# Kernel optimization log

Measured on AMD Instinct MI355X. Metric: run time of the kernel, lower is better.

## Reference

```python
import jax, jax.numpy as jnp
import numpy as np

B, L, J, D_MODEL, N_HIDDEN = 8, 2048, 2048, 1024, 1024


def setup_inputs() -> dict:
    key = jax.random.key(0)
    ks = jax.random.split(key, 6)
    scale = 1.0 / np.sqrt(D_MODEL)
    return {
        "q": jax.random.normal(ks[0], (B, L, D_MODEL), dtype=jnp.float32),
        "k": jax.random.normal(ks[1], (B, J, D_MODEL), dtype=jnp.float32),
        "v": jax.random.normal(ks[2], (B, J, D_MODEL), dtype=jnp.float32),
        "mask": jnp.zeros((B, L, J), dtype=jnp.float32),
        # Linear(d_model, n_hidden, bias=False) weights, stored [n_hidden, d_model] like torch
        "W_q": jax.random.normal(ks[3], (N_HIDDEN, D_MODEL), dtype=jnp.float32) * scale,
        "W_k": jax.random.normal(ks[4], (N_HIDDEN, D_MODEL), dtype=jnp.float32) * scale,
        "W_v": jax.random.normal(ks[5], (N_HIDDEN, D_MODEL), dtype=jnp.float32) * scale,
    }


def reference(q, k, v, mask, W_q, W_k, W_v):
    # Linear projections (torch Linear: x @ W.T)
    qp = jnp.einsum('bld,hd->blh', q, W_q)
    kp = jnp.einsum('bjd,hd->bjh', k, W_k)
    vp = jnp.einsum('bjd,hd->bjh', v, W_v)
    # scaled dot-product scores [B, L, J]
    scores = jnp.einsum('blh,bjh->blj', qp, kp) / jnp.sqrt(jnp.float32(N_HIDDEN)).astype(qp.dtype)
    scores = scores + mask
    attn = jax.nn.softmax(scores, axis=-1)
    return jnp.einsum('blj,bjh->blh', attn, vp)
```

## Files before the change

kernel.cpp:

```cpp
#include <hip/hip_runtime.h>
#include <hip/hip_fp16.h>

typedef _Float16 f16;
typedef __attribute__((ext_vector_type(8))) _Float16 f16x8;
typedef __attribute__((ext_vector_type(4))) _Float16 f16x4;
typedef __attribute__((ext_vector_type(4))) float f32x4;

#define BM 256
#define BN 256
#define BK 32

__device__ __forceinline__ void gll16(const void* src, void* dst) {
  __builtin_amdgcn_global_load_lds((const __attribute__((address_space(1))) void*)src,
                                   (__attribute__((address_space(3))) void*)dst,
                                   16, 0, 0);
}

template<int MODE>
__global__ __launch_bounds__(512, 2)
void gemm_bt(const f16* __restrict__ Aall, const f16* __restrict__ Ball,
             void* __restrict__ Call,
             int M, int N, int K, int lda, int ldb, int ldc,
             long strideA, long strideB, long strideC,
             const float* __restrict__ maskAll, long strideMask,
             float* __restrict__ lvec, float scale)
{
  __shared__ f16 smA[3][BM * BK];
  __shared__ f16 smB[3][BN * BK];

  const int z = blockIdx.z;
  const f16* A = Aall + (long)z * strideA;
  const f16* B = Ball + (long)z * strideB;

  const int tid  = threadIdx.x;
  const int wid  = tid >> 6;
  const int lane = tid & 63;
  const int wm = wid >> 2;
  const int wn = wid & 3;
  const int lr = lane & 15;
  const int g  = lane >> 4;
  const int xc = (lr & 3) ^ ((lr >> 2) & 3);

  const long brow = (long)blockIdx.y * BM;
  const long bcol = (long)blockIdx.x * BN;
  const int  nt   = K / BK;

  f32x4 acc[8][4] = {};

  auto stageA = [&](int buf, int t) {
    #pragma unroll
    for (int i = 0; i < 2; ++i) {
      int c   = i * 512 + tid;
      int row = c >> 2;
      int sl  = (c & 3) ^ ((row & 3) ^ ((row >> 2) & 3));
      gll16(A + (brow + row) * (long)lda + t * BK + sl * 8, &smA[buf][c * 8]);
    }
  };
  auto stageB = [&](int buf, int t) {
    #pragma unroll
    for (int i = 0; i < 2; ++i) {
      int c   = i * 512 + tid;
      int row = c >> 2;
      int sl  = (c & 3) ^ ((row & 3) ^ ((row >> 2) & 3));
      gll16(B + (bcol + row) * (long)ldb + t * BK + sl * 8, &smB[buf][c * 8]);
    }
  };

  stageA(0, 0); stageB(0, 0);
  stageA(1, 1); stageB(1, 1);
  asm volatile("s_waitcnt vmcnt(4)" ::: "memory");
  __builtin_amdgcn_s_barrier();

  int buf = 0;
  for (int kt = 0; kt < nt; ++kt) {
    int bufn = buf + 2; if (bufn >= 3) bufn -= 3;
    const f16* sa = &smA[buf][0];
    const f16* sb = &smB[buf][0];

    f16x8 af[4], bf[4];
    #pragma unroll
    for (int n = 0; n < 4; ++n) {
      int row = wn * 64 + n * 16 + lr;
      bf[n] = *(const f16x8*)(sb + row * BK + (g ^ xc) * 8);
    }
    #pragma unroll
    for (int m = 0; m < 4; ++m) {
      int row = wm * 128 + m * 16 + lr;
      af[m] = *(const f16x8*)(sa + row * BK + (g ^ xc) * 8);
    }
    if (kt + 2 < nt) stageA(bufn, kt + 2);
    __builtin_amdgcn_s_barrier();
    asm volatile("s_waitcnt lgkmcnt(0)" ::: "memory");
    __builtin_amdgcn_sched_barrier(0);
    __builtin_amdgcn_s_setprio(1);
    #pragma unroll
    for (int m = 0; m < 4; ++m)
      #pragma unroll
      for (int n = 0; n < 4; ++n)
        acc[m][n] = __builtin_amdgcn_mfma_f32_16x16x32_f16(af[m], bf[n], acc[m][n], 0, 0, 0);
    __builtin_amdgcn_s_setprio(0);
    __builtin_amdgcn_s_barrier();

    #pragma unroll
    for (int m = 0; m < 4; ++m) {
      int row = wm * 128 + 64 + m * 16 + lr;
      af[m] = *(const f16x8*)(sa + row * BK + (g ^ xc) * 8);
    }
    if (kt + 2 < nt) stageB(bufn, kt + 2);
    __builtin_amdgcn_s_barrier();
    asm volatile("s_waitcnt lgkmcnt(0)" ::: "memory");
    __builtin_amdgcn_sched_barrier(0);
    __builtin_amdgcn_s_setprio(1);
    #pragma unroll
    for (int m = 0; m < 4; ++m)
      #pragma unroll
      for (int n = 0; n < 4; ++n)
        acc[m + 4][n] = __builtin_amdgcn_mfma_f32_16x16x32_f16(af[m], bf[n], acc[m + 4][n], 0, 0, 0);
    __builtin_amdgcn_s_setprio(0);
    __builtin_amdgcn_sched_barrier(0);
    if (kt + 2 < nt) { asm volatile("s_waitcnt vmcnt(4)" ::: "memory"); }
    else             { asm volatile("s_waitcnt vmcnt(0)" ::: "memory"); }
    __builtin_amdgcn_s_barrier();
    buf = buf + 1 == 3 ? 0 : buf + 1;
  }

  const int rb = (lane >> 4) * 4;

  if (MODE == 0) {
    f16* C = (f16*)Call + (long)z * strideC;
    #pragma unroll
    for (int m = 0; m < 8; ++m)
      #pragma unroll
      for (int j = 0; j < 4; ++j) {
        long grow = brow + wm * 128 + m * 16 + rb + j;
        #pragma unroll
        for (int n = 0; n < 4; ++n) {
          long gcol = bcol + wn * 64 + n * 16 + lr;
          C[grow * ldc + gcol] = (f16)acc[m][n][j];
        }
      }
  } else if (MODE == 1) {
    f16* C = (f16*)Call + (long)z * strideC;
    const float* mask = maskAll + (long)z * strideMask;
    #pragma unroll
    for (int m = 0; m < 8; ++m)
      #pragma unroll
      for (int j = 0; j < 4; ++j) {
        long grow = brow + wm * 128 + m * 16 + rb + j;
        float s = 0.f;
        #pragma unroll
        for (int n = 0; n < 4; ++n) {
          long gcol = bcol + wn * 64 + n * 16 + lr;
          float p = __expf(acc[m][n][j] * scale + mask[grow * ldc + gcol]);
          C[grow * ldc + gcol] = (f16)p;
          s += p;
        }
        s += __shfl_xor(s, 1);
        s += __shfl_xor(s, 2);
        s += __shfl_xor(s, 4);
        s += __shfl_xor(s, 8);
        if (lr == 0)
          lvec[((long)z * M + grow) * 32 + blockIdx.x * 4 + wn] = s;
      }
  } else {
    float* C = (float*)Call + (long)z * strideC;
    #pragma unroll
    for (int m = 0; m < 8; ++m)
      #pragma unroll
      for (int j = 0; j < 4; ++j) {
        long grow = brow + wm * 128 + m * 16 + rb + j;
        float inv = 1.0f / lvec[(long)z * M + grow];
        #pragma unroll
        for (int n = 0; n < 4; ++n) {
          long gcol = bcol + wn * 64 + n * 16 + lr;
          C[grow * ldc + gcol] = acc[m][n][j] * inv;
        }
      }
  }
}

__global__ void cvt_f32_to_f16(const float* __restrict__ src, f16* __restrict__ dst, int n4) {
  int i = blockIdx.x * blockDim.x + threadIdx.x;
  if (i < n4) {
    float4 vv = ((const float4*)src)[i];
    f16x4 o;
    o[0] = (f16)vv.x; o[1] = (f16)vv.y; o[2] = (f16)vv.z; o[3] = (f16)vv.w;
    ((f16x4*)dst)[i] = o;
  }
}

__global__ void reduce_l(const float* __restrict__ lpart, float* __restrict__ lsum, int n) {
  int i = blockIdx.x * blockDim.x + threadIdx.x;
  if (i < n) {
    float s = 0.f;
    #pragma unroll
    for (int j = 0; j < 32; ++j) s += lpart[(long)i * 32 + j];
    lsum[i] = s;
  }
}

extern "C" void kernel_launch(void* const* d_in, const int* in_sizes, int n_in,
                              void* d_out, int out_size, void* d_ws, size_t ws_size,
                              hipStream_t stream)
{
  const int Bb = 8, L = 2048, J = 2048, D = 1024, H = 1024;
  const float* q    = (const float*)d_in[0];
  const float* k    = (const float*)d_in[1];
  const float* v    = (const float*)d_in[2];
  const float* mask = (const float*)d_in[3];
  const float* Wq   = (const float*)d_in[4];
  const float* Wk   = (const float*)d_in[5];
  const float* Wv   = (const float*)d_in[6];
  float* out = (float*)d_out;
  char*  ws  = (char*)d_ws;

  f16* qf  = (f16*)(ws + 0);
  f16* kf  = (f16*)(ws + 33554432);
  f16* vf  = (f16*)(ws + 67108864);
  f16* Pm  = (f16*)(ws + 0);
  f16* Wqf = (f16*)(ws + 100663296);
  f16* Wkf = (f16*)(ws + 102760448);
  f16* Wvf = (f16*)(ws + 104857600);
  f16* qp  = (f16*)(ws + 106954752);
  f16* kp  = (f16*)(ws + 140509184);
  f16* vpT = (f16*)(ws + 174063616);
  float* lpart = (float*)(ws + 207618048);
  float* lsum  = (float*)(ws + 209715200);

  const long nQ = (long)Bb * L * D;
  const long nW = (long)H * D;

  cvt_f32_to_f16<<<dim3((unsigned)(nQ / 4 / 256)), dim3(256), 0, stream>>>(q, qf, (int)(nQ / 4));
  cvt_f32_to_f16<<<dim3((unsigned)(nQ / 4 / 256)), dim3(256), 0, stream>>>(k, kf, (int)(nQ / 4));
  cvt_f32_to_f16<<<dim3((unsigned)(nQ / 4 / 256)), dim3(256), 0, stream>>>(v, vf, (int)(nQ / 4));
  cvt_f32_to_f16<<<dim3((unsigned)(nW / 4 / 256)), dim3(256), 0, stream>>>(Wq, Wqf, (int)(nW / 4));
  cvt_f32_to_f16<<<dim3((unsigned)(nW / 4 / 256)), dim3(256), 0, stream>>>(Wk, Wkf, (int)(nW / 4));
  cvt_f32_to_f16<<<dim3((unsigned)(nW / 4 / 256)), dim3(256), 0, stream>>>(Wv, Wvf, (int)(nW / 4));

  gemm_bt<0><<<dim3(1024 / BN, 16384 / BM, 1), dim3(512), 0, stream>>>(
      qf, Wqf, qp, 16384, 1024, 1024, 1024, 1024, 1024,
      0, 0, 0, nullptr, 0, nullptr, 0.f);
  gemm_bt<0><<<dim3(1024 / BN, 16384 / BM, 1), dim3(512), 0, stream>>>(
      kf, Wkf, kp, 16384, 1024, 1024, 1024, 1024, 1024,
      0, 0, 0, nullptr, 0, nullptr, 0.f);
  gemm_bt<0><<<dim3(2048 / BN, 1024 / BM, 8), dim3(512), 0, stream>>>(
      Wvf, vf, vpT, 1024, 2048, 1024, 1024, 1024, 2048,
      0, (long)J * D, (long)H * J, nullptr, 0, nullptr, 0.f);

  gemm_bt<1><<<dim3(2048 / BN, 2048 / BM, 8), dim3(512), 0, stream>>>(
      qp, kp, Pm, 2048, 2048, 1024, 1024, 1024, 2048,
      (long)L * H, (long)J * H, (long)L * J, mask, (long)L * J, lpart, 0.03125f);

  reduce_l<<<dim3(16384 / 256), dim3(256), 0, stream>>>(lpart, lsum, 16384);

  gemm_bt<2><<<dim3(1024 / BN, 2048 / BM, 8), dim3(512), 0, stream>>>(
      Pm, vpT, out, 2048, 1024, 2048, 2048, 2048, 1024,
      (long)L * J, (long)H * J, (long)L * H, nullptr, 0, lsum, 0.f);
}
```

Baseline: 411.6 us.

## Switch GEMM to double-buffered BK=64 pipeline and fuse input conversions

```diff
diff --git a/kernel.cpp b/kernel.cpp
--- a/kernel.cpp
+++ b/kernel.cpp
@@ -8,7 +8,7 @@
 
 #define BM 256
 #define BN 256
-#define BK 32
+#define BK 64
 
 __device__ __forceinline__ void gll16(const void* src, void* dst) {
   __builtin_amdgcn_global_load_lds((const __attribute__((address_space(1))) void*)src,
@@ -25,8 +25,8 @@
              const float* __restrict__ maskAll, long strideMask,
              float* __restrict__ lvec, float scale)
 {
-  __shared__ f16 smA[3][BM * BK];
-  __shared__ f16 smB[3][BN * BK];
+  __shared__ __align__(16) f16 smA[2][BM * BK];
+  __shared__ __align__(16) f16 smB[2][BN * BK];
 
   const int z = blockIdx.z;
   const f16* A = Aall + (long)z * strideA;
@@ -39,7 +39,6 @@
   const int wn = wid & 3;
   const int lr = lane & 15;
   const int g  = lane >> 4;
-  const int xc = (lr & 3) ^ ((lr >> 2) & 3);
 
   const long brow = (long)blockIdx.y * BM;
   const long bcol = (long)blockIdx.x * BN;
@@ -47,48 +46,44 @@
 
   f32x4 acc[8][4] = {};
 
-  auto stageA = [&](int buf, int t) {
-    #pragma unroll
-    for (int i = 0; i < 2; ++i) {
-      int c   = i * 512 + tid;
-      int row = c >> 2;
-      int sl  = (c & 3) ^ ((row & 3) ^ ((row >> 2) & 3));
+  auto stA = [&](int buf, int t, int i0) {
+    #pragma unroll
+    for (int ii = 0; ii < 2; ++ii) {
+      int c   = (i0 + ii) * 512 + tid;
+      int row = c >> 3;
+      int sl  = (c & 7) ^ (row & 7);
       gll16(A + (brow + row) * (long)lda + t * BK + sl * 8, &smA[buf][c * 8]);
     }
   };
-  auto stageB = [&](int buf, int t) {
-    #pragma unroll
-    for (int i = 0; i < 2; ++i) {
-      int c   = i * 512 + tid;
-      int row = c >> 2;
-      int sl  = (c & 3) ^ ((row & 3) ^ ((row >> 2) & 3));
+  auto stB = [&](int buf, int t, int i0) {
+    #pragma unroll
+    for (int ii = 0; ii < 2; ++ii) {
+      int c   = (i0 + ii) * 512 + tid;
+      int row = c >> 3;
+      int sl  = (c & 7) ^ (row & 7);
       gll16(B + (bcol + row) * (long)ldb + t * BK + sl * 8, &smB[buf][c * 8]);
     }
   };
-
-  stageA(0, 0); stageB(0, 0);
-  stageA(1, 1); stageB(1, 1);
-  asm volatile("s_waitcnt vmcnt(4)" ::: "memory");
+  auto ld = [&](const f16* base, int r, int ks) -> f16x8 {
+    return *(const f16x8*)(base + r * BK + (((ks << 2) + g) ^ (r & 7)) * 8);
+  };
+
+  stA(0, 0, 0); stA(0, 0, 2); stB(0, 0, 0); stB(0, 0, 2);
+  asm volatile("s_waitcnt vmcnt(0)" ::: "memory");
   __builtin_amdgcn_s_barrier();
 
-  int buf = 0;
   for (int kt = 0; kt < nt; ++kt) {
-    int bufn = buf + 2; if (bufn >= 3) bufn -= 3;
-    const f16* sa = &smA[buf][0];
-    const f16* sb = &smB[buf][0];
-
+    const int cur = kt & 1;
+    const f16* sa = smA[cur];
+    const f16* sb = smB[cur];
+    const bool pf = (kt + 1 < nt);
     f16x8 af[4], bf[4];
-    #pragma unroll
-    for (int n = 0; n < 4; ++n) {
-      int row = wn * 64 + n * 16 + lr;
-      bf[n] = *(const f16x8*)(sb + row * BK + (g ^ xc) * 8);
-    }
-    #pragma unroll
-    for (int m = 0; m < 4; ++m) {
-      int row = wm * 128 + m * 16 + lr;
-      af[m] = *(const f16x8*)(sa + row * BK + (g ^ xc) * 8);
-    }
-    if (kt + 2 < nt) stageA(bufn, kt + 2);
+
+    #pragma unroll
+    for (int n = 0; n < 4; ++n) bf[n] = ld(sb, wn * 64 + n * 16 + lr, 0);
+    #pragma unroll
+    for (int m = 0; m < 4; ++m) af[m] = ld(sa, wm * 128 + m * 16 + lr, 0);
+    if (pf) { stA(cur ^ 1, kt + 1, 0); stA(cur ^ 1, kt + 1, 2); }
     __builtin_amdgcn_s_barrier();
     asm volatile("s_waitcnt lgkmcnt(0)" ::: "memory");
     __builtin_amdgcn_sched_barrier(0);
@@ -102,11 +97,8 @@
     __builtin_amdgcn_s_barrier();
 
     #pragma unroll
-    for (int m = 0; m < 4; ++m) {
-      int row = wm * 128 + 64 + m * 16 + lr;
-      af[m] = *(const f16x8*)(sa + row * BK + (g ^ xc) * 8);
-    }
-    if (kt + 2 < nt) stageB(bufn, kt + 2);
+    for (int m = 0; m < 4; ++m) af[m] = ld(sa, wm * 128 + 64 + m * 16 + lr, 0);
+    if (pf) { stB(cur ^ 1, kt + 1, 0); stB(cur ^ 1, kt + 1, 2); }
     __builtin_amdgcn_s_barrier();
     asm volatile("s_waitcnt lgkmcnt(0)" ::: "memory");
     __builtin_amdgcn_sched_barrier(0);
@@ -117,11 +109,39 @@
       for (int n = 0; n < 4; ++n)
         acc[m + 4][n] = __builtin_amdgcn_mfma_f32_16x16x32_f16(af[m], bf[n], acc[m + 4][n], 0, 0, 0);
     __builtin_amdgcn_s_setprio(0);
-    __builtin_amdgcn_sched_barrier(0);
-    if (kt + 2 < nt) { asm volatile("s_waitcnt vmcnt(4)" ::: "memory"); }
-    else             { asm volatile("s_waitcnt vmcnt(0)" ::: "memory"); }
-    __builtin_amdgcn_s_barrier();
-    buf = buf + 1 == 3 ? 0 : buf + 1;
+    __builtin_amdgcn_s_barrier();
+
+    #pragma unroll
+    for (int n = 0; n < 4; ++n) bf[n] = ld(sb, wn * 64 + n * 16 + lr, 1);
+    #pragma unroll
+    for (int m = 0; m < 4; ++m) af[m] = ld(sa, wm * 128 + m * 16 + lr, 1);
+    __builtin_amdgcn_s_barrier();
+    asm volatile("s_waitcnt lgkmcnt(0)" ::: "memory");
+    __builtin_amdgcn_sched_barrier(0);
+    __builtin_amdgcn_s_setprio(1);
+    #pragma unroll
+    for (int m = 0; m < 4; ++m)
+      #pragma unroll
+      for (int n = 0; n < 4; ++n)
+        acc[m][n] = __builtin_amdgcn_mfma_f32_16x16x32_f16(af[m], bf[n], acc[m][n], 0, 0, 0);
+    __builtin_amdgcn_s_setprio(0);
+    __builtin_amdgcn_s_barrier();
+
+    #pragma unroll
+    for (int m = 0; m < 4; ++m) af[m] = ld(sa, wm * 128 + 64 + m * 16 + lr, 1);
+    __builtin_amdgcn_s_barrier();
+    asm volatile("s_waitcnt lgkmcnt(0)" ::: "memory");
+    __builtin_amdgcn_sched_barrier(0);
+    __builtin_amdgcn_s_setprio(1);
+    #pragma unroll
+    for (int m = 0; m < 4; ++m)
+      #pragma unroll
+      for (int n = 0; n < 4; ++n)
+        acc[m + 4][n] = __builtin_amdgcn_mfma_f32_16x16x32_f16(af[m], bf[n], acc[m + 4][n], 0, 0, 0);
+    __builtin_amdgcn_s_setprio(0);
+    __builtin_amdgcn_sched_barrier(0);
+    asm volatile("s_waitcnt vmcnt(0)" ::: "memory");
+    __builtin_amdgcn_s_barrier();
   }
 
   const int rb = (lane >> 4) * 4;
@@ -179,13 +199,27 @@
   }
 }
 
-__global__ void cvt_f32_to_f16(const float* __restrict__ src, f16* __restrict__ dst, int n4) {
-  int i = blockIdx.x * blockDim.x + threadIdx.x;
-  if (i < n4) {
-    float4 vv = ((const float4*)src)[i];
+__global__ void cvt_all(const float* __restrict__ q, const float* __restrict__ k,
+                        const float* __restrict__ v, const float* __restrict__ Wq,
+                        const float* __restrict__ Wk, const float* __restrict__ Wv,
+                        f16* __restrict__ qf, f16* __restrict__ kf, f16* __restrict__ vf,
+                        f16* __restrict__ Wqf, f16* __restrict__ Wkf, f16* __restrict__ Wvf)
+{
+  const long NQ4 = 4194304, NW4 = 262144;
+  const long total = 3 * NQ4 + 3 * NW4;
+  for (long i = (long)blockIdx.x * blockDim.x + threadIdx.x; i < total;
+       i += (long)gridDim.x * blockDim.x) {
+    const float* src; f16* dst; long j = i;
+    if      (j <     NQ4)           { src = q;  dst = qf; }
+    else if (j < 2 * NQ4)           { src = k;  dst = kf;  j -= NQ4; }
+    else if (j < 3 * NQ4)           { src = v;  dst = vf;  j -= 2 * NQ4; }
+    else if (j < 3 * NQ4 + NW4)     { src = Wq; dst = Wqf; j -= 3 * NQ4; }
+    else if (j < 3 * NQ4 + 2 * NW4) { src = Wk; dst = Wkf; j -= 3 * NQ4 + NW4; }
+    else                            { src = Wv; dst = Wvf; j -= 3 * NQ4 + 2 * NW4; }
+    float4 vv = ((const float4*)src)[j];
     f16x4 o;
     o[0] = (f16)vv.x; o[1] = (f16)vv.y; o[2] = (f16)vv.z; o[3] = (f16)vv.w;
-    ((f16x4*)dst)[i] = o;
+    ((f16x4*)dst)[j] = o;
   }
 }
 
@@ -203,7 +237,6 @@
                               void* d_out, int out_size, void* d_ws, size_t ws_size,
                               hipStream_t stream)
 {
-  const int Bb = 8, L = 2048, J = 2048, D = 1024, H = 1024;
   const float* q    = (const float*)d_in[0];
   const float* k    = (const float*)d_in[1];
   const float* v    = (const float*)d_in[2];
@@ -227,15 +260,9 @@
   float* lpart = (float*)(ws + 207618048);
   float* lsum  = (float*)(ws + 209715200);
 
-  const long nQ = (long)Bb * L * D;
-  const long nW = (long)H * D;
-
-  cvt_f32_to_f16<<<dim3((unsigned)(nQ / 4 / 256)), dim3(256), 0, stream>>>(q, qf, (int)(nQ / 4));
-  cvt_f32_to_f16<<<dim3((unsigned)(nQ / 4 / 256)), dim3(256), 0, stream>>>(k, kf, (int)(nQ / 4));
-  cvt_f32_to_f16<<<dim3((unsigned)(nQ / 4 / 256)), dim3(256), 0, stream>>>(v, vf, (int)(nQ / 4));
-  cvt_f32_to_f16<<<dim3((unsigned)(nW / 4 / 256)), dim3(256), 0, stream>>>(Wq, Wqf, (int)(nW / 4));
-  cvt_f32_to_f16<<<dim3((unsigned)(nW / 4 / 256)), dim3(256), 0, stream>>>(Wk, Wkf, (int)(nW / 4));
-  cvt_f32_to_f16<<<dim3((unsigned)(nW / 4 / 256)), dim3(256), 0, stream>>>(Wv, Wvf, (int)(nW / 4));
+  const long L = 2048, J = 2048, D = 1024, H = 1024;
+
+  cvt_all<<<dim3(2048), dim3(256), 0, stream>>>(q, k, v, Wq, Wk, Wv, qf, kf, vf, Wqf, Wkf, Wvf);
 
   gemm_bt<0><<<dim3(1024 / BN, 16384 / BM, 1), dim3(512), 0, stream>>>(
       qf, Wqf, qp, 16384, 1024, 1024, 1024, 1024, 1024,
@@ -245,15 +272,15 @@
       0, 0, 0, nullptr, 0, nullptr, 0.f);
   gemm_bt<0><<<dim3(2048 / BN, 1024 / BM, 8), dim3(512), 0, stream>>>(
       Wvf, vf, vpT, 1024, 2048, 1024, 1024, 1024, 2048,
-      0, (long)J * D, (long)H * J, nullptr, 0, nullptr, 0.f);
+      0, J * D, H * J, nullptr, 0, nullptr, 0.f);
 
   gemm_bt<1><<<dim3(2048 / BN, 2048 / BM, 8), dim3(512), 0, stream>>>(
       qp, kp, Pm, 2048, 2048, 1024, 1024, 1024, 2048,
-      (long)L * H, (long)J * H, (long)L * J, mask, (long)L * J, lpart, 0.03125f);
+      L * H, J * H, L * J, mask, L * J, lpart, 0.03125f);
 
   reduce_l<<<dim3(16384 / 256), dim3(256), 0, stream>>>(lpart, lsum, 16384);
 
   gemm_bt<2><<<dim3(1024 / BN, 2048 / BM, 8), dim3(512), 0, stream>>>(
       Pm, vpT, out, 2048, 1024, 2048, 2048, 2048, 1024,
-      (long)L * J, (long)H * J, (long)L * H, nullptr, 0, lsum, 0.f);
-}
+      L * J, H * J, L * H, nullptr, 0, lsum, 0.f);
+}
```

Measured after the change: 380.6 us. -7.5%, faster.
